# Kernel optimization log

Measured on AMD Instinct MI355X. Metric: run time of the kernel, lower is better.

The kernel has to match this reference:

```python
import jax, jax.numpy as jnp
import numpy as np

BETA = 0.25


def setup_inputs() -> dict:
    key = jax.random.key(0)
    k1, k2 = jax.random.split(key)
    B, T, D, K = 16, 4096, 256, 4096
    z_e = jax.random.normal(k1, (B, T, D), dtype=jnp.float32)
    # emulate uniform(-1/K, 1/K) init but any values work for correctness
    codebook = jax.random.uniform(k2, (K, D), dtype=jnp.float32,
                                  minval=-1.0 / K, maxval=1.0 / K)
    return {"z_e": z_e, "codebook": codebook}


def reference(z_e, codebook):
    D = codebook.shape[1]
    z_flat = z_e.reshape(-1, D)                                  # [N, D]
    # squared L2 distances: ||z||^2 + ||e||^2 - 2 z.e
    z_norm = jnp.sum(z_flat ** 2, axis=1, keepdims=True)          # [N, 1]
    e_norm = jnp.sum(codebook ** 2, axis=1)                       # [K]
    dist = z_norm + e_norm - 2.0 * jnp.matmul(z_flat, codebook.T) # [N, K]
    idx_flat = jnp.argmin(dist, axis=1)                           # [N]
    idx = idx_flat.reshape(z_e.shape[:-1])                        # [B, T]
    z_q = codebook[idx]                                           # [B, T, D]
    # commitment loss: beta * mse(stop_grad(z_q), z_e)
    loss = BETA * jnp.mean((jax.lax.stop_gradient(z_q) - z_e) ** 2)
    # straight-through estimator
    z_q_st = z_e + jax.lax.stop_gradient(z_q - z_e)
    return z_q_st, idx, loss
```

## Files before the change

### kernel.cpp

```cpp
#include <hip/hip_runtime.h>
#include <cfloat>

#define NROWS 65536
#define DIM   256
#define KCB   4096

#define EPS_WIN  1.8e-4f
#define CAND_CAP 16

typedef __attribute__((ext_vector_type(8))) short short8;
typedef __attribute__((ext_vector_type(4))) float f32x4;

__global__ void norms_kernel(const float* __restrict__ x, float* __restrict__ out) {
  const int row  = blockIdx.x * 4 + (threadIdx.x >> 6);
  const int lane = threadIdx.x & 63;
  const float4 v = ((const float4*)(x + (size_t)row * DIM))[lane];
  float s = v.x * v.x + v.y * v.y + v.z * v.z + v.w * v.w;
  #pragma unroll
  for (int off = 32; off > 0; off >>= 1) s += __shfl_down(s, off);
  if (lane == 0) out[row] = s;
}

__device__ inline unsigned short f2bf(float x) {
  unsigned int u = __float_as_uint(x);
  return (unsigned short)((u + 0x7fffu + ((u >> 16) & 1u)) >> 16);
}

__global__ void prep_kernel(const float* __restrict__ z, const float* __restrict__ cb,
                            unsigned short* __restrict__ zh, unsigned short* __restrict__ eh) {
  const long long j = (long long)blockIdx.x * 256 + threadIdx.x;
  const long long NZ8 = (long long)NROWS * DIM / 8;
  const float* src; unsigned short* dst; long long base;
  if (j < NZ8) { src = z;  dst = zh; base = j * 8; }
  else         { src = cb; dst = eh; base = (j - NZ8) * 8; }
  const float4 v0 = *(const float4*)(src + base);
  const float4 v1 = *(const float4*)(src + base + 4);
  union { unsigned short us[8]; uint4 u4; } o;
  o.us[0] = f2bf(v0.x); o.us[1] = f2bf(v0.y); o.us[2] = f2bf(v0.z); o.us[3] = f2bf(v0.w);
  o.us[4] = f2bf(v1.x); o.us[5] = f2bf(v1.y); o.us[6] = f2bf(v1.z); o.us[7] = f2bf(v1.w);
  *(uint4*)(dst + base) = o.u4;
}

__launch_bounds__(256, 2)
__global__ void screen_kernel(const unsigned short* __restrict__ zh,
                              const unsigned short* __restrict__ eh,
                              const float* __restrict__ znorm,
                              const float* __restrict__ enorm,
                              unsigned int* __restrict__ counts,
                              unsigned short* __restrict__ cands) {
  __shared__ __align__(16) unsigned short a_s[128 * 256];
  __shared__ __align__(16) unsigned short b_s[128 * 32];
  __shared__ float zn_s[128];
  __shared__ unsigned int cnt_s[128];
  __shared__ unsigned short cand_s[128 * CAND_CAP];

  const int tid = threadIdx.x;
  const int wv  = tid >> 6;
  const int ln  = tid & 63;
  const int l15 = ln & 15;
  const int lg  = ln >> 4;
  const int rbase = blockIdx.x * 128;

  if (tid < 128) { zn_s[tid] = znorm[rbase + tid]; cnt_s[tid] = 0u; }

  #pragma unroll 1
  for (int i = 0; i < 16; ++i) {
    const int gid = i * 256 + tid;
    const int row = gid >> 5, slot = gid & 31;
    const int sw  = slot ^ (row & 7);
    *(uint4*)(&a_s[row * 256 + sw * 8]) =
        *(const uint4*)(&zh[(size_t)(rbase + row) * 256 + slot * 8]);
  }
  __syncthreads();

  float znv[8];
  #pragma unroll
  for (int fr = 0; fr < 2; ++fr)
    #pragma unroll
    for (int q = 0; q < 4; ++q)
      znv[fr * 4 + q] = zn_s[wv * 32 + fr * 16 + lg * 4 + q];

  float rm[8];
  #pragma unroll
  for (int s = 0; s < 8; ++s) rm[s] = FLT_MAX;

  #pragma unroll 1
  for (int kt = 0; kt < KCB / 128; ++kt) {
    const int kcb0 = kt * 128;
    f32x4 acc[2][8];
    #pragma unroll
    for (int fr = 0; fr < 2; ++fr)
      #pragma unroll
      for (int fc = 0; fc < 8; ++fc)
        acc[fr][fc] = (f32x4){0.f, 0.f, 0.f, 0.f};

    #pragma unroll 1
    for (int dc = 0; dc < 8; ++dc) {
      __syncthreads();
      #pragma unroll
      for (int i = 0; i < 2; ++i) {
        const int c  = i * 64 + wv * 16 + l15;
        const int sw = lg ^ ((c >> 1) & 3);
        *(uint4*)(&b_s[c * 32 + sw * 8]) =
            *(const uint4*)(&eh[(size_t)(kcb0 + c) * 256 + dc * 32 + lg * 8]);
      }
      __syncthreads();

      short8 af[2];
      #pragma unroll
      for (int fr = 0; fr < 2; ++fr) {
        const int r = wv * 32 + fr * 16 + l15;
        const int sl = (dc * 4 + lg) ^ (r & 7);
        af[fr] = *(const short8*)(&a_s[r * 256 + sl * 8]);
      }
      short8 bf[8];
      #pragma unroll
      for (int fc = 0; fc < 8; ++fc) {
        const int c = fc * 16 + l15;
        const int sw = lg ^ ((c >> 1) & 3);
        bf[fc] = *(const short8*)(&b_s[c * 32 + sw * 8]);
      }
      #pragma unroll
      for (int fr = 0; fr < 2; ++fr)
        #pragma unroll
        for (int fc = 0; fc < 8; ++fc)
          acc[fr][fc] = __builtin_amdgcn_mfma_f32_16x16x32_bf16(
              af[fr], bf[fc], acc[fr][fc], 0, 0, 0);
    }

    float en_[8];
    #pragma unroll
    for (int fc = 0; fc < 8; ++fc) en_[fc] = enorm[kcb0 + fc * 16 + l15];

    float tm[8];
    #pragma unroll
    for (int s = 0; s < 8; ++s) tm[s] = FLT_MAX;

    #pragma unroll
    for (int fr = 0; fr < 2; ++fr)
      #pragma unroll
      for (int fc = 0; fc < 8; ++fc)
        #pragma unroll
        for (int q = 0; q < 4; ++q) {
          const float d_ = fmaf(-2.0f, acc[fr][fc][q], znv[fr * 4 + q] + en_[fc]);
          tm[fr * 4 + q] = fminf(tm[fr * 4 + q], d_);
        }

    float th[8];
    #pragma unroll
    for (int s = 0; s < 8; ++s) {
      float v = tm[s];
      v = fminf(v, __shfl_xor(v, 1));
      v = fminf(v, __shfl_xor(v, 2));
      v = fminf(v, __shfl_xor(v, 4));
      v = fminf(v, __shfl_xor(v, 8));
      const float m = fminf(rm[s], v);
      rm[s] = m;
      th[s] = m + EPS_WIN;
    }

    #pragma unroll
    for (int fr = 0; fr < 2; ++fr)
      #pragma unroll
      for (int fc = 0; fc < 8; ++fc)
        #pragma unroll
        for (int q = 0; q < 4; ++q) {
          const float d_ = fmaf(-2.0f, acc[fr][fc][q], znv[fr * 4 + q] + en_[fc]);
          if (d_ <= th[fr * 4 + q]) {
            const int rl = wv * 32 + fr * 16 + lg * 4 + q;
            const unsigned int pos = atomicAdd(&cnt_s[rl], 1u);
            if (pos < CAND_CAP)
              cand_s[rl * CAND_CAP + pos] = (unsigned short)(kcb0 + fc * 16 + l15);
          }
        }
  }

  __syncthreads();
  if (tid < 128) counts[rbase + tid] = cnt_s[tid];
  for (int i = tid; i < 128 * CAND_CAP; i += 256)
    cands[(size_t)rbase * CAND_CAP + i] = cand_s[i];
}

__global__ void rescore_kernel(const float* __restrict__ z, const float* __restrict__ cb,
                               const float* __restrict__ znorm, const float* __restrict__ enorm,
                               const unsigned int* __restrict__ counts,
                               const unsigned short* __restrict__ cands,
                               int* __restrict__ idx) {
  const int gw  = (blockIdx.x * 256 + threadIdx.x) >> 6;
  const int ln  = threadIdx.x & 63;
  const int row = gw * 4 + (ln >> 4);
  const int ci  = ln & 15;
  const unsigned int cnt = counts[row];

  float bv = FLT_MAX; int bk = 0x7fffffff;
  if (cnt <= CAND_CAP) {
    const int active = ci < (int)cnt;
    const int k = active ? (int)cands[(size_t)row * CAND_CAP + ci] : 0;
    const float* zr = z  + (size_t)row * DIM;
    const float* er = cb + (size_t)k   * DIM;
    float acc = 0.0f;
    #pragma unroll 8
    for (int d = 0; d < DIM; ++d) acc = fmaf(zr[d], er[d], acc);
    const float dist = fmaf(-2.0f, acc, znorm[row] + enorm[k]);
    if (active) { bv = dist; bk = k; }
  }
  #pragma unroll
  for (int off = 1; off < 16; off <<= 1) {
    const float ov = __shfl_xor(bv, off);
    const int   ok = __shfl_xor(bk, off);
    if (ov < bv || (ov == bv && ok < bk)) { bv = ov; bk = ok; }
  }
  if (ci == 0 && cnt <= CAND_CAP) idx[row] = bk;
}

__global__ void fallback_kernel(const float* __restrict__ z, const float* __restrict__ cb,
                                const float* __restrict__ znorm, const float* __restrict__ enorm,
                                const unsigned int* __restrict__ counts,
                                int* __restrict__ idx) {
  __shared__ float bd_s[256];
  __shared__ int   bk_s[256];
  const int tid = threadIdx.x;
  for (int row = blockIdx.x; row < NROWS; row += gridDim.x) {
    if (counts[row] <= CAND_CAP) continue;
    const float zn = znorm[row];
    const float* zr = z + (size_t)row * DIM;
    float bv = FLT_MAX; int bk = 0x7fffffff;
    for (int k = tid; k < KCB; k += 256) {
      const float* er = cb + (size_t)k * DIM;
      float acc = 0.0f;
      #pragma unroll 8
      for (int d = 0; d < DIM; ++d) acc = fmaf(zr[d], er[d], acc);
      const float dist = fmaf(-2.0f, acc, zn + enorm[k]);
      if (dist < bv || (dist == bv && k < bk)) { bv = dist; bk = k; }
    }
    bd_s[tid] = bv; bk_s[tid] = bk;
    __syncthreads();
    for (int s = 128; s > 0; s >>= 1) {
      if (tid < s) {
        const float ov = bd_s[tid + s]; const int ok = bk_s[tid + s];
        if (ov < bd_s[tid] || (ov == bd_s[tid] && ok < bk_s[tid])) {
          bd_s[tid] = ov; bk_s[tid] = ok;
        }
      }
      __syncthreads();
    }
    if (tid == 0) idx[row] = bk_s[0];
    __syncthreads();
  }
}

#define BM 128
#define BK 128
#define BD 32
#define LSTR 36
__launch_bounds__(256, 2)
__global__ void argmin_kernel(const float* __restrict__ z,
                              const float* __restrict__ cb,
                              const float* __restrict__ znorm,
                              const float* __restrict__ enorm,
                              int* __restrict__ idx_out) {
  __shared__ float z_s[BM * LSTR];
  __shared__ float e_s[BK * LSTR];
  __shared__ float zn_s[BM];
  const int tid = threadIdx.x;
  const int tx = tid & 15;
  const int ty = tid >> 4;
  const int rbase = blockIdx.x * BM;
  if (tid < BM) zn_s[tid] = znorm[rbase + tid];
  float bestv[8]; int besti[8];
  #pragma unroll
  for (int i = 0; i < 8; ++i) { bestv[i] = FLT_MAX; besti[i] = 0; }
  for (int kc = 0; kc < KCB; kc += BK) {
    float acc[8][8];
    #pragma unroll
    for (int i = 0; i < 8; ++i)
      #pragma unroll
      for (int j = 0; j < 8; ++j) acc[i][j] = 0.0f;
    for (int dc = 0; dc < DIM; dc += BD) {
      __syncthreads();
      #pragma unroll
      for (int p = 0; p < 4; ++p) {
        const int el = p * 256 + tid;
        const int r  = el >> 3;
        const int c4 = (el & 7) * 4;
        *(float4*)(&z_s[r * LSTR + c4]) =
            *(const float4*)(z + (size_t)(rbase + r) * DIM + dc + c4);
        *(float4*)(&e_s[r * LSTR + c4]) =
            *(const float4*)(cb + (size_t)(kc + r) * DIM + dc + c4);
      }
      __syncthreads();
      #pragma unroll 1
      for (int dd = 0; dd < BD; dd += 4) {
        float4 b[8];
        #pragma unroll
        for (int j = 0; j < 8; ++j)
          b[j] = *(const float4*)(&e_s[(tx + 16 * j) * LSTR + dd]);
        #pragma unroll
        for (int i = 0; i < 8; ++i) {
          const float4 a = *(const float4*)(&z_s[(ty + 16 * i) * LSTR + dd]);
          #pragma unroll
          for (int j = 0; j < 8; ++j)
            acc[i][j] += a.x * b[j].x + a.y * b[j].y + a.z * b[j].z + a.w * b[j].w;
        }
      }
    }
    float en[8];
    #pragma unroll
    for (int j = 0; j < 8; ++j) en[j] = enorm[kc + tx + 16 * j];
    #pragma unroll
    for (int i = 0; i < 8; ++i) {
      const float zn = zn_s[ty + 16 * i];
      #pragma unroll
      for (int j = 0; j < 8; ++j) {
        const float t1 = zn + en[j];
        const float dist = t1 - 2.0f * acc[i][j];
        const int k = kc + tx + 16 * j;
        if (dist < bestv[i]) { bestv[i] = dist; besti[i] = k; }
      }
    }
  }
  #pragma unroll
  for (int i = 0; i < 8; ++i) {
    float lv = bestv[i]; int li = besti[i];
    #pragma unroll
    for (int off = 1; off < 16; off <<= 1) {
      const float ov = __shfl_xor(lv, off);
      const int   oi = __shfl_xor(li, off);
      if (ov < lv || (ov == lv && oi < li)) { lv = ov; li = oi; }
    }
    if (tx == 0) idx_out[rbase + ty + 16 * i] = li;
  }
}

__global__ void gather_kernel(const float* __restrict__ z,
                              const float* __restrict__ cb,
                              const int* __restrict__ idx,
                              float* __restrict__ out_zq,
                              float* __restrict__ out_idx,
                              float* __restrict__ partials) {
  const int row  = blockIdx.x * 4 + (threadIdx.x >> 6);
  const int lane = threadIdx.x & 63;
  const int k = idx[row];
  const float4 zv = ((const float4*)(z  + (size_t)row * DIM))[lane];
  const float4 ev = ((const float4*)(cb + (size_t)k   * DIM))[lane];
  float4 d, st;
  d.x = ev.x - zv.x; d.y = ev.y - zv.y; d.z = ev.z - zv.z; d.w = ev.w - zv.w;
  st.x = zv.x + d.x; st.y = zv.y + d.y; st.z = zv.z + d.z; st.w = zv.w + d.w;
  ((float4*)(out_zq + (size_t)row * DIM))[lane] = st;
  if (lane == 0) out_idx[row] = (float)k;
  float s = d.x * d.x + d.y * d.y + d.z * d.z + d.w * d.w;
  #pragma unroll
  for (int off = 32; off > 0; off >>= 1) s += __shfl_down(s, off);
  __shared__ float ps[4];
  if (lane == 0) ps[threadIdx.x >> 6] = s;
  __syncthreads();
  if (threadIdx.x == 0)
    partials[blockIdx.x] = (ps[0] + ps[1]) + (ps[2] + ps[3]);
}

__global__ void loss_kernel(const float* __restrict__ partials,
                            float* __restrict__ out_loss) {
  float s = 0.0f;
  for (int i = threadIdx.x; i < NROWS / 4; i += 256) s += partials[i];
  #pragma unroll
  for (int off = 32; off > 0; off >>= 1) s += __shfl_down(s, off);
  __shared__ float ps[4];
  if ((threadIdx.x & 63) == 0) ps[threadIdx.x >> 6] = s;
  __syncthreads();
  if (threadIdx.x == 0)
    *out_loss = 0.25f * (((ps[0] + ps[1]) + (ps[2] + ps[3])) *
                         (1.0f / (float)((size_t)NROWS * DIM)));
}

extern "C" void kernel_launch(void* const* d_in, const int* in_sizes, int n_in,
                              void* d_out, int out_size, void* d_ws, size_t ws_size,
                              hipStream_t stream) {
  const float* z  = (const float*)d_in[0];
  const float* cb = (const float*)d_in[1];

  float* out_zq   = (float*)d_out;
  float* out_idx  = out_zq + (size_t)NROWS * DIM;
  float* out_loss = out_idx + NROWS;

  char* w = (char*)d_ws;
  unsigned short* zh    = (unsigned short*)(w);
  unsigned short* eh    = (unsigned short*)(w + 33554432);
  float* enorm          = (float*)(w + 35651584);
  float* znorm          = (float*)(w + 35667968);
  int*   idx            = (int*)(w + 35930112);
  unsigned int* counts  = (unsigned int*)(w + 36192256);
  unsigned short* cands = (unsigned short*)(w + 36454400);
  float* partials       = (float*)(w + 38551552);
  const size_t NEED = 38617088;

  if (ws_size >= NEED) {
    hipLaunchKernelGGL(norms_kernel, dim3(KCB / 4), dim3(256), 0, stream, cb, enorm);
    hipLaunchKernelGGL(norms_kernel, dim3(NROWS / 4), dim3(256), 0, stream, z, znorm);
    hipLaunchKernelGGL(prep_kernel, dim3((NROWS * DIM / 8 + KCB * DIM / 8) / 256),
                       dim3(256), 0, stream, z, cb, zh, eh);
    hipLaunchKernelGGL(screen_kernel, dim3(NROWS / 128), dim3(256), 0, stream,
                       zh, eh, znorm, enorm, counts, cands);
    hipLaunchKernelGGL(rescore_kernel, dim3(NROWS / 16), dim3(256), 0, stream,
                       z, cb, znorm, enorm, counts, cands, idx);
    hipLaunchKernelGGL(fallback_kernel, dim3(256), dim3(256), 0, stream,
                       z, cb, znorm, enorm, counts, idx);
    hipLaunchKernelGGL(gather_kernel, dim3(NROWS / 4), dim3(256), 0, stream,
                       z, cb, idx, out_zq, out_idx, partials);
    hipLaunchKernelGGL(loss_kernel, dim3(1), dim3(256), 0, stream, partials, out_loss);
  } else {
    float* ws        = (float*)d_ws;
    float* enorm_l   = ws;
    float* znorm_l   = ws + KCB;
    int*   idx_l     = (int*)(ws + KCB + NROWS);
    float* partials_l= ws + KCB + 2 * NROWS;
    hipLaunchKernelGGL(norms_kernel, dim3(KCB / 4), dim3(256), 0, stream, cb, enorm_l);
    hipLaunchKernelGGL(norms_kernel, dim3(NROWS / 4), dim3(256), 0, stream, z, znorm_l);
    hipLaunchKernelGGL(argmin_kernel, dim3(NROWS / BM), dim3(256), 0, stream,
                       z, cb, znorm_l, enorm_l, idx_l);
    hipLaunchKernelGGL(gather_kernel, dim3(NROWS / 4), dim3(256), 0, stream,
                       z, cb, idx_l, out_zq, out_idx, partials_l);
    hipLaunchKernelGGL(loss_kernel, dim3(1), dim3(256), 0, stream, partials_l, out_loss);
  }
}
```

Baseline: 474.3 us.

## Fuse norms into bf16 prep, retile screen warps 2x2, skip candidate scan

```diff
diff --git a/kernel.cpp b/kernel.cpp
--- a/kernel.cpp
+++ b/kernel.cpp
@@ -11,34 +11,27 @@
 typedef __attribute__((ext_vector_type(8))) short short8;
 typedef __attribute__((ext_vector_type(4))) float f32x4;
 
-__global__ void norms_kernel(const float* __restrict__ x, float* __restrict__ out) {
-  const int row  = blockIdx.x * 4 + (threadIdx.x >> 6);
-  const int lane = threadIdx.x & 63;
-  const float4 v = ((const float4*)(x + (size_t)row * DIM))[lane];
-  float s = v.x * v.x + v.y * v.y + v.z * v.z + v.w * v.w;
-  #pragma unroll
-  for (int off = 32; off > 0; off >>= 1) s += __shfl_down(s, off);
-  if (lane == 0) out[row] = s;
-}
-
 __device__ inline unsigned short f2bf(float x) {
   unsigned int u = __float_as_uint(x);
   return (unsigned short)((u + 0x7fffu + ((u >> 16) & 1u)) >> 16);
 }
 
-__global__ void prep_kernel(const float* __restrict__ z, const float* __restrict__ cb,
-                            unsigned short* __restrict__ zh, unsigned short* __restrict__ eh) {
-  const long long j = (long long)blockIdx.x * 256 + threadIdx.x;
-  const long long NZ8 = (long long)NROWS * DIM / 8;
-  const float* src; unsigned short* dst; long long base;
-  if (j < NZ8) { src = z;  dst = zh; base = j * 8; }
-  else         { src = cb; dst = eh; base = (j - NZ8) * 8; }
-  const float4 v0 = *(const float4*)(src + base);
-  const float4 v1 = *(const float4*)(src + base + 4);
-  union { unsigned short us[8]; uint4 u4; } o;
-  o.us[0] = f2bf(v0.x); o.us[1] = f2bf(v0.y); o.us[2] = f2bf(v0.z); o.us[3] = f2bf(v0.w);
-  o.us[4] = f2bf(v1.x); o.us[5] = f2bf(v1.y); o.us[6] = f2bf(v1.z); o.us[7] = f2bf(v1.w);
-  *(uint4*)(dst + base) = o.u4;
+__global__ void prep_norms_kernel(const float* __restrict__ z, const float* __restrict__ cb,
+                                  unsigned short* __restrict__ zh, unsigned short* __restrict__ eh,
+                                  float* __restrict__ znorm, float* __restrict__ enorm) {
+  const int r    = blockIdx.x * 4 + (threadIdx.x >> 6);
+  const int lane = threadIdx.x & 63;
+  const float* src; unsigned short* dst; float* nrm; int row;
+  if (r < NROWS) { src = z;  dst = zh; nrm = znorm; row = r; }
+  else           { src = cb; dst = eh; nrm = enorm; row = r - NROWS; }
+  const float4 v = ((const float4*)(src + (size_t)row * DIM))[lane];
+  union { unsigned short us[4]; uint2 u2; } o;
+  o.us[0] = f2bf(v.x); o.us[1] = f2bf(v.y); o.us[2] = f2bf(v.z); o.us[3] = f2bf(v.w);
+  *(uint2*)(dst + (size_t)row * DIM + lane * 4) = o.u2;
+  float s = v.x * v.x + v.y * v.y + v.z * v.z + v.w * v.w;
+  #pragma unroll
+  for (int off = 32; off > 0; off >>= 1) s += __shfl_down(s, off);
+  if (lane == 0) nrm[row] = s;
 }
 
 __launch_bounds__(256, 2)
@@ -59,6 +52,8 @@
   const int ln  = tid & 63;
   const int l15 = ln & 15;
   const int lg  = ln >> 4;
+  const int wr  = wv >> 1;
+  const int wc  = wv & 1;
   const int rbase = blockIdx.x * 128;
 
   if (tid < 128) { zn_s[tid] = znorm[rbase + tid]; cnt_s[tid] = 0u; }
@@ -73,25 +68,25 @@
   }
   __syncthreads();
 
-  float znv[8];
-  #pragma unroll
-  for (int fr = 0; fr < 2; ++fr)
+  float znv[16];
+  #pragma unroll
+  for (int fr = 0; fr < 4; ++fr)
     #pragma unroll
     for (int q = 0; q < 4; ++q)
-      znv[fr * 4 + q] = zn_s[wv * 32 + fr * 16 + lg * 4 + q];
-
-  float rm[8];
-  #pragma unroll
-  for (int s = 0; s < 8; ++s) rm[s] = FLT_MAX;
+      znv[fr * 4 + q] = zn_s[wr * 64 + fr * 16 + lg * 4 + q];
+
+  float rm[16];
+  #pragma unroll
+  for (int s = 0; s < 16; ++s) rm[s] = FLT_MAX;
 
   #pragma unroll 1
   for (int kt = 0; kt < KCB / 128; ++kt) {
     const int kcb0 = kt * 128;
-    f32x4 acc[2][8];
-    #pragma unroll
-    for (int fr = 0; fr < 2; ++fr)
-      #pragma unroll
-      for (int fc = 0; fc < 8; ++fc)
+    f32x4 acc[4][4];
+    #pragma unroll
+    for (int fr = 0; fr < 4; ++fr)
+      #pragma unroll
+      for (int fc = 0; fc < 4; ++fc)
         acc[fr][fc] = (f32x4){0.f, 0.f, 0.f, 0.f};
 
     #pragma unroll 1
@@ -106,49 +101,50 @@
       }
       __syncthreads();
 
-      short8 af[2];
-      #pragma unroll
-      for (int fr = 0; fr < 2; ++fr) {
-        const int r = wv * 32 + fr * 16 + l15;
+      short8 af[4];
+      #pragma unroll
+      for (int fr = 0; fr < 4; ++fr) {
+        const int r = wr * 64 + fr * 16 + l15;
         const int sl = (dc * 4 + lg) ^ (r & 7);
         af[fr] = *(const short8*)(&a_s[r * 256 + sl * 8]);
       }
-      short8 bf[8];
-      #pragma unroll
-      for (int fc = 0; fc < 8; ++fc) {
-        const int c = fc * 16 + l15;
+      short8 bf[4];
+      #pragma unroll
+      for (int fc = 0; fc < 4; ++fc) {
+        const int c = wc * 64 + fc * 16 + l15;
         const int sw = lg ^ ((c >> 1) & 3);
         bf[fc] = *(const short8*)(&b_s[c * 32 + sw * 8]);
       }
       #pragma unroll
-      for (int fr = 0; fr < 2; ++fr)
+      for (int fr = 0; fr < 4; ++fr)
         #pragma unroll
-        for (int fc = 0; fc < 8; ++fc)
+        for (int fc = 0; fc < 4; ++fc)
           acc[fr][fc] = __builtin_amdgcn_mfma_f32_16x16x32_bf16(
               af[fr], bf[fc], acc[fr][fc], 0, 0, 0);
     }
 
-    float en_[8];
-    #pragma unroll
-    for (int fc = 0; fc < 8; ++fc) en_[fc] = enorm[kcb0 + fc * 16 + l15];
-
-    float tm[8];
-    #pragma unroll
-    for (int s = 0; s < 8; ++s) tm[s] = FLT_MAX;
-
-    #pragma unroll
-    for (int fr = 0; fr < 2; ++fr)
-      #pragma unroll
-      for (int fc = 0; fc < 8; ++fc)
+    float en_[4];
+    #pragma unroll
+    for (int fc = 0; fc < 4; ++fc) en_[fc] = enorm[kcb0 + wc * 64 + fc * 16 + l15];
+
+    float tm[16];
+    #pragma unroll
+    for (int s = 0; s < 16; ++s) tm[s] = FLT_MAX;
+
+    #pragma unroll
+    for (int fr = 0; fr < 4; ++fr)
+      #pragma unroll
+      for (int fc = 0; fc < 4; ++fc)
         #pragma unroll
         for (int q = 0; q < 4; ++q) {
           const float d_ = fmaf(-2.0f, acc[fr][fc][q], znv[fr * 4 + q] + en_[fc]);
           tm[fr * 4 + q] = fminf(tm[fr * 4 + q], d_);
         }
 
-    float th[8];
-    #pragma unroll
-    for (int s = 0; s < 8; ++s) {
+    float th[16];
+    float guard = 1.0f;
+    #pragma unroll
+    for (int s = 0; s < 16; ++s) {
       float v = tm[s];
       v = fminf(v, __shfl_xor(v, 1));
       v = fminf(v, __shfl_xor(v, 2));
@@ -157,22 +153,26 @@
       const float m = fminf(rm[s], v);
       rm[s] = m;
       th[s] = m + EPS_WIN;
-    }
-
-    #pragma unroll
-    for (int fr = 0; fr < 2; ++fr)
-      #pragma unroll
-      for (int fc = 0; fc < 8; ++fc)
+      guard = fminf(guard, tm[s] - th[s]);
+    }
+
+    if (__any(guard <= 0.0f)) {
+      #pragma unroll
+      for (int fr = 0; fr < 4; ++fr)
         #pragma unroll
-        for (int q = 0; q < 4; ++q) {
-          const float d_ = fmaf(-2.0f, acc[fr][fc][q], znv[fr * 4 + q] + en_[fc]);
-          if (d_ <= th[fr * 4 + q]) {
-            const int rl = wv * 32 + fr * 16 + lg * 4 + q;
-            const unsigned int pos = atomicAdd(&cnt_s[rl], 1u);
-            if (pos < CAND_CAP)
-              cand_s[rl * CAND_CAP + pos] = (unsigned short)(kcb0 + fc * 16 + l15);
+        for (int fc = 0; fc < 4; ++fc)
+          #pragma unroll
+          for (int q = 0; q < 4; ++q) {
+            const float d_ = fmaf(-2.0f, acc[fr][fc][q], znv[fr * 4 + q] + en_[fc]);
+            if (d_ <= th[fr * 4 + q]) {
+              const int rl = wr * 64 + fr * 16 + lg * 4 + q;
+              const unsigned int pos = atomicAdd(&cnt_s[rl], 1u);
+              if (pos < CAND_CAP)
+                cand_s[rl * CAND_CAP + pos] =
+                    (unsigned short)(kcb0 + wc * 64 + fc * 16 + l15);
+            }
           }
-        }
+    }
   }
 
   __syncthreads();
@@ -196,11 +196,16 @@
   if (cnt <= CAND_CAP) {
     const int active = ci < (int)cnt;
     const int k = active ? (int)cands[(size_t)row * CAND_CAP + ci] : 0;
-    const float* zr = z  + (size_t)row * DIM;
-    const float* er = cb + (size_t)k   * DIM;
-    float acc = 0.0f;
-    #pragma unroll 8
-    for (int d = 0; d < DIM; ++d) acc = fmaf(zr[d], er[d], acc);
+    const float4* zr = (const float4*)(z  + (size_t)row * DIM);
+    const float4* er = (const float4*)(cb + (size_t)k   * DIM);
+    float ax = 0.f, ay = 0.f, az = 0.f, aw = 0.f;
+    #pragma unroll 4
+    for (int d = 0; d < DIM / 4; ++d) {
+      const float4 zv = zr[d], ev = er[d];
+      ax = fmaf(zv.x, ev.x, ax); ay = fmaf(zv.y, ev.y, ay);
+      az = fmaf(zv.z, ev.z, az); aw = fmaf(zv.w, ev.w, aw);
+    }
+    const float acc = (ax + ay) + (az + aw);
     const float dist = fmaf(-2.0f, acc, znorm[row] + enorm[k]);
     if (active) { bv = dist; bk = k; }
   }
@@ -249,6 +254,16 @@
   }
 }
 
+__global__ void norms_kernel(const float* __restrict__ x, float* __restrict__ out) {
+  const int row  = blockIdx.x * 4 + (threadIdx.x >> 6);
+  const int lane = threadIdx.x & 63;
+  const float4 v = ((const float4*)(x + (size_t)row * DIM))[lane];
+  float s = v.x * v.x + v.y * v.y + v.z * v.z + v.w * v.w;
+  #pragma unroll
+  for (int off = 32; off > 0; off >>= 1) s += __shfl_down(s, off);
+  if (lane == 0) out[row] = s;
+}
+
 #define BM 128
 #define BK 128
 #define BD 32
@@ -394,10 +409,8 @@
   const size_t NEED = 38617088;
 
   if (ws_size >= NEED) {
-    hipLaunchKernelGGL(norms_kernel, dim3(KCB / 4), dim3(256), 0, stream, cb, enorm);
-    hipLaunchKernelGGL(norms_kernel, dim3(NROWS / 4), dim3(256), 0, stream, z, znorm);
-    hipLaunchKernelGGL(prep_kernel, dim3((NROWS * DIM / 8 + KCB * DIM / 8) / 256),
-                       dim3(256), 0, stream, z, cb, zh, eh);
+    hipLaunchKernelGGL(prep_norms_kernel, dim3((NROWS + KCB) / 4), dim3(256), 0, stream,
+                       z, cb, zh, eh, znorm, enorm);
     hipLaunchKernelGGL(screen_kernel, dim3(NROWS / 128), dim3(256), 0, stream,
                        zh, eh, znorm, enorm, counts, cands);
     hipLaunchKernelGGL(rescore_kernel, dim3(NROWS / 16), dim3(256), 0, stream,
```

Result: slower. 1.292 ms (+172.5%).
